# Performance work log

Hardware: AMD Instinct MI355X
Metric: run time of the kernel (lower is better)

The kernel has to match this reference:

```python
import jax, jax.numpy as jnp
import numpy as np

H = 8  # num_heads


def setup_inputs() -> dict:
    key = jax.random.key(0)
    ks = jax.random.split(key, 8)
    B, N, C = 2048, 64, 256  # B = batch(8) * nW(256) windows, N = window tokens, C = dim
    nW = 256
    return {
        "x": jax.random.normal(ks[0], (B, N, C), jnp.float32),
        "mask": jax.random.normal(ks[1], (nW, N, N), jnp.float32),
        "Wq": jax.random.normal(ks[2], (C, C), jnp.float32) * (C ** -0.5),
        "bq": jax.random.normal(ks[3], (C,), jnp.float32) * 0.02,
        "Wkv": jax.random.normal(ks[4], (C, 2 * C), jnp.float32) * (C ** -0.5),
        "bkv": jax.random.normal(ks[5], (2 * C,), jnp.float32) * 0.02,
        "Wp": jax.random.normal(ks[6], (C, C), jnp.float32) * (C ** -0.5),
        "bp": jax.random.normal(ks[7], (C,), jnp.float32) * 0.02,
    }


def reference(x, mask, Wq, bq, Wkv, bkv, Wp, bp):
    B, N, C = x.shape
    dh = C // H
    scale = dh ** -0.5
    # projections (attn_kv is None -> self-attention)
    q = (x @ Wq + bq).reshape(B, N, H, dh).transpose(0, 2, 1, 3)          # [B,H,N,dh]
    kv = (x @ Wkv + bkv).reshape(B, N, 2, H, dh).transpose(2, 0, 3, 1, 4)  # [2,B,H,N,dh]
    k, v = kv[0], kv[1]
    attn = jnp.einsum("bhqd,bhkd->bhqk", q * scale, k)                    # [B,H,N,N]
    nW = mask.shape[0]
    attn = attn.reshape(B // nW, nW, H, N, N) + mask[None, :, None]
    attn = attn.reshape(B, H, N, N)
    attn = jax.nn.softmax(attn, axis=-1)
    out = jnp.einsum("bhqk,bhkd->bhqd", attn, v)                          # [B,H,N,dh]
    out = out.transpose(0, 2, 1, 3).reshape(B, N, C)
    return out @ Wp + bp
```

## Files before the change

kernel.cpp:

```cpp
#include <hip/hip_runtime.h>

typedef __bf16 bf16v8 __attribute__((ext_vector_type(8)));
typedef bf16v8 bf16x8 __attribute__((may_alias));
typedef unsigned int u32v2 __attribute__((ext_vector_type(2)));
typedef u32v2 u32x2 __attribute__((may_alias));
typedef unsigned short u16v8 __attribute__((ext_vector_type(8)));
typedef u16v8 u16x8 __attribute__((may_alias));
typedef unsigned short u16v;
typedef u16v u16 __attribute__((may_alias));
typedef _Float16 f16v4 __attribute__((ext_vector_type(4)));
typedef f16v4 f16x4 __attribute__((may_alias));
typedef _Float16 f16v;
typedef f16v f16s __attribute__((may_alias));
typedef float f32x4 __attribute__((ext_vector_type(4)));
typedef unsigned int u32;

#define MEMFENCE() asm volatile("" ::: "memory")

union B8 { u32 u[4]; bf16v8 v; };

__device__ __forceinline__ u32 cvtpk(float lo, float hi) {
    u32 r;
    asm("v_cvt_pk_bf16_f32 %0, %1, %2" : "=v"(r) : "v"(lo), "v"(hi));
    return r;
}

__device__ __forceinline__ unsigned short f2b(float f) {
    union { float f; unsigned u; } a; a.f = f;
    unsigned r = a.u + 0x7FFFu + ((a.u >> 16) & 1u);
    return (unsigned short)(r >> 16);
}

__global__ void prep_weights(const float* __restrict__ Wq,
                             const float* __restrict__ Wkv,
                             const float* __restrict__ Wp,
                             const float* __restrict__ bq,
                             const float* __restrict__ bkv,
                             u16* __restrict__ wt,
                             u16* __restrict__ wpt,
                             float* __restrict__ b_all)
{
    int idx = blockIdx.x * 256 + threadIdx.x;
    if (idx < 196608) {
        int h  = idx / 24576;   int r  = idx % 24576;
        int m  = r / 8192;      int r2 = r % 8192;
        int tj = r2 / 4096;     int r3 = r2 % 4096;
        int ks = r3 / 512;      int r4 = r3 % 512;
        int lane = r4 >> 3, j = r4 & 7;
        int o = h * 32 + tj * 16 + (lane & 15);
        int k = ks * 32 + (lane >> 4) * 8 + j;
        float v = (m == 0) ? Wq[k * 256 + o]
                           : Wkv[k * 512 + (m == 1 ? o : 256 + o)];
        wt[idx] = f2b(v);
    } else if (idx < 262144) {
        int f  = idx - 196608;
        int h  = f / 8192;      int r2 = f % 8192;
        int tj = r2 / 4096;     int r3 = r2 % 4096;
        int ks = r3 / 512;      int r4 = r3 % 512;
        int lane = r4 >> 3, j = r4 & 7;
        int o = h * 32 + tj * 16 + (lane & 15);
        int k = ks * 32 + (lane >> 4) * 8 + j;
        wpt[f] = f2b(Wp[k * 256 + o]);
    } else if (idx < 262912) {
        int i = idx - 262144;
        b_all[i] = (i < 256) ? bq[i] : bkv[i - 256];
    }
}

__global__ __launch_bounds__(512, 2)
void qkv_proj(const float* __restrict__ x,
              const u16* __restrict__ wt,
              const float* __restrict__ b_all,
              u16* __restrict__ qkv)
{
    __shared__ __align__(16) unsigned char smem[65536];
    const int b0  = blockIdx.x * 2;
    const int tid = threadIdx.x;
    const int w   = tid >> 6;
    const int l   = tid & 63;
    const int lr  = l & 15;
    const int lg  = l >> 4;
    const int hc  = w * 32;

    f32x4 zero = {0.f, 0.f, 0.f, 0.f};

#pragma unroll
    for (int it = 0; it < 8; ++it) {
        int g   = it * 512 + tid;
        int win = g >> 11;
        int r2  = g & 2047;
        int row = r2 >> 5;
        int cg  = r2 & 31;
        const float* xb = x + (size_t)(b0 + win) * 16384;
        const float4 f0 = *(const float4*)(xb + row * 256 + cg * 8);
        const float4 f1 = *(const float4*)(xb + row * 256 + cg * 8 + 4);
        u16v8 t;
        t[0] = f2b(f0.x); t[1] = f2b(f0.y); t[2] = f2b(f0.z); t[3] = f2b(f0.w);
        t[4] = f2b(f1.x); t[5] = f2b(f1.y); t[6] = f2b(f1.z); t[7] = f2b(f1.w);
        int off = win * 32768 + row * 512 + ((cg * 16) ^ ((row & 7) << 4));
        *(u16x8*)(smem + off) = t;
    }
    __syncthreads();

    const u16* whead = wt + (size_t)w * 24576;

#pragma unroll
    for (int hf = 0; hf < 2; ++hf) {
#pragma unroll
        for (int m = 0; m < 3; ++m) {
            f32x4 acc[2][2][2];
#pragma unroll
            for (int win = 0; win < 2; ++win)
#pragma unroll
                for (int t = 0; t < 2; ++t)
#pragma unroll
                    for (int tj = 0; tj < 2; ++tj) acc[win][t][tj] = zero;
#pragma unroll
            for (int ks = 0; ks < 8; ++ks) {
                bf16v8 wf[2];
#pragma unroll
                for (int tj = 0; tj < 2; ++tj)
                    wf[tj] = *(const bf16x8*)(whead + m * 8192 + tj * 4096 + ks * 512 + l * 8);
#pragma unroll
                for (int win = 0; win < 2; ++win)
#pragma unroll
                    for (int t = 0; t < 2; ++t) {
                        int row = hf * 32 + t * 16 + lr;
                        bf16v8 af = *(const bf16x8*)(smem + win * 32768 + row * 512 +
                                                     ((ks * 64 + lg * 16) ^ ((row & 7) << 4)));
                        __builtin_amdgcn_s_setprio(1);
#pragma unroll
                        for (int tj = 0; tj < 2; ++tj)
                            acc[win][t][tj] = __builtin_amdgcn_mfma_f32_16x16x32_bf16(af, wf[tj], acc[win][t][tj], 0, 0, 0);
                        __builtin_amdgcn_s_setprio(0);
                    }
            }
#pragma unroll
            for (int win = 0; win < 2; ++win) {
                u16* base = qkv + (((size_t)(b0 + win) * 8 + w) * 3) * 2048 + m * 2048;
#pragma unroll
                for (int tj = 0; tj < 2; ++tj) {
                    float bias = b_all[m * 256 + hc + tj * 16 + lr];
#pragma unroll
                    for (int t = 0; t < 2; ++t) {
                        if (m < 2) {
#pragma unroll
                            for (int e = 0; e < 4; ++e) {
                                int tok = hf * 32 + t * 16 + lg * 4 + e;
                                base[tok * 32 + tj * 16 + lr] = f2b(acc[win][t][tj][e] + bias);
                            }
                        } else {
                            int dh   = tj * 16 + lr;
                            int tok0 = hf * 32 + t * 16 + lg * 4;
                            u32x2 pv2;
                            pv2[0] = cvtpk(acc[win][t][tj][0] + bias, acc[win][t][tj][1] + bias);
                            pv2[1] = cvtpk(acc[win][t][tj][2] + bias, acc[win][t][tj][3] + bias);
                            *(u32x2*)((unsigned char*)base + dh * 128 + tok0 * 2) = pv2;
                        }
                    }
                }
            }
        }
    }
}

__global__ __launch_bounds__(512, 4)
void attn_out(const u16* __restrict__ qkv,
              const float* __restrict__ mask,
              const u16* __restrict__ wpt,
              const float* __restrict__ bp,
              float* __restrict__ out)
{
    __shared__ __align__(16) unsigned char smem[40960];
    const int b   = blockIdx.x;
    const int wdw = b & 255;
    const int tid = threadIdx.x;
    const int w   = tid >> 6;
    const int l   = tid & 63;
    const int lr  = l & 15;
    const int lg  = l >> 4;
    const int chunk = w * 4096;
    const int moff  = 32768;
    const int hc    = w * 32;
    const float scale = 0.17677669529663687f;

    f32x4 zero = {0.f, 0.f, 0.f, 0.f};

    {
        const float* mb = mask + (size_t)wdw * 4096;
#pragma unroll
        for (int it = 0; it < 8; ++it) {
            int idx = it * 512 + tid;
            int q = idx >> 6, k = idx & 63;
            int colp = (k & 15) * 4 + (k >> 4);
            *(f16s*)(smem + moff + q * 128 + ((colp * 2) ^ ((q & 7) << 4)))
                = (_Float16)mb[idx];
        }
    }
    __syncthreads();

    const u16* qb  = qkv + (((size_t)b * 8 + w) * 3) * 2048;
    const u16* kb_ = qb + 2048;
    const unsigned char* vb = (const unsigned char*)(qb + 4096);

    bf16v8 aq[4], bk[4];
#pragma unroll
    for (int ti = 0; ti < 4; ++ti)
        aq[ti] = *(const bf16x8*)(qb + (ti * 16 + lr) * 32 + lg * 8);
#pragma unroll
    for (int tj = 0; tj < 4; ++tj)
        bk[tj] = *(const bf16x8*)(kb_ + (tj * 16 + lr) * 32 + lg * 8);

    f32x4 sH[4][4];
    __builtin_amdgcn_s_setprio(1);
#pragma unroll
    for (int ti = 0; ti < 4; ++ti)
#pragma unroll
        for (int tj = 0; tj < 4; ++tj)
            sH[ti][tj] = __builtin_amdgcn_mfma_f32_16x16x32_bf16(aq[ti], bk[tj], zero, 0, 0, 0);
    __builtin_amdgcn_s_setprio(0);

#pragma unroll
    for (int ti = 0; ti < 4; ++ti)
#pragma unroll
        for (int e = 0; e < 4; ++e) {
            int row = ti * 16 + lg * 4 + e;
            f16v4 mv = *(const f16x4*)(smem + moff + row * 128 + ((lr * 8) ^ ((row & 7) << 4)));
#pragma unroll
            for (int tj = 0; tj < 4; ++tj)
                sH[ti][tj][e] = sH[ti][tj][e] * scale + (float)mv[tj];
        }
    float inv[4][4];
#pragma unroll
    for (int ti = 0; ti < 4; ++ti)
#pragma unroll
        for (int e = 0; e < 4; ++e) {
            float v0 = sH[ti][0][e], v1 = sH[ti][1][e];
            float v2 = sH[ti][2][e], v3 = sH[ti][3][e];
            float m = fmaxf(fmaxf(v0, v1), fmaxf(v2, v3));
#pragma unroll
            for (int d = 1; d < 16; d <<= 1) m = fmaxf(m, __shfl_xor(m, d));
            v0 = __expf(v0 - m); v1 = __expf(v1 - m);
            v2 = __expf(v2 - m); v3 = __expf(v3 - m);
            float s = v0 + v1 + v2 + v3;
#pragma unroll
            for (int d = 1; d < 16; d <<= 1) s += __shfl_xor(s, d);
            inv[ti][e] = 1.0f / s;
            sH[ti][0][e] = v0; sH[ti][1][e] = v1;
            sH[ti][2][e] = v2; sH[ti][3][e] = v3;
        }
    u32 pkP[4][4][2];
#pragma unroll
    for (int ti = 0; ti < 4; ++ti)
#pragma unroll
        for (int tj = 0; tj < 4; ++tj) {
            pkP[ti][tj][0] = cvtpk(sH[ti][tj][0], sH[ti][tj][1]);
            pkP[ti][tj][1] = cvtpk(sH[ti][tj][2], sH[ti][tj][3]);
        }

    f32x4 oH[4][2];
#pragma unroll
    for (int ti = 0; ti < 4; ++ti)
#pragma unroll
        for (int tjv = 0; tjv < 2; ++tjv) oH[ti][tjv] = zero;
#pragma unroll
    for (int kb2 = 0; kb2 < 2; ++kb2) {
#pragma unroll
        for (int ti = 0; ti < 4; ++ti)
#pragma unroll
            for (int tjh = 0; tjh < 2; ++tjh) {
                int c2 = (tjh * 16 + lr) * 2;
#pragma unroll
                for (int ep = 0; ep < 2; ++ep) {
                    u32 u = pkP[ti][2 * kb2 + tjh][ep];
                    int q0 = ti * 16 + lg * 4 + ep * 2;
                    *(u16*)(smem + chunk + q0 * 64 + (c2 ^ (((q0 >> 1) & 3) << 4))) = (unsigned short)u;
                    *(u16*)(smem + chunk + (q0 + 1) * 64 + (c2 ^ ((((q0 + 1) >> 1) & 3) << 4))) = (unsigned short)(u >> 16);
                }
            }
        MEMFENCE();
        bf16v8 bv[2];
#pragma unroll
        for (int tjv = 0; tjv < 2; ++tjv) {
            int dh = tjv * 16 + lr;
            bv[tjv] = *(const bf16x8*)(vb + dh * 128 + kb2 * 64 + lg * 16);
        }
#pragma unroll
        for (int ti = 0; ti < 4; ++ti) {
            int row = ti * 16 + lr;
            bf16v8 ap = *(const bf16x8*)(smem + chunk + row * 64 + ((lg * 16) ^ (((row >> 1) & 3) << 4)));
            __builtin_amdgcn_s_setprio(1);
#pragma unroll
            for (int tjv = 0; tjv < 2; ++tjv)
                oH[ti][tjv] = __builtin_amdgcn_mfma_f32_16x16x32_bf16(ap, bv[tjv], oH[ti][tjv], 0, 0, 0);
            __builtin_amdgcn_s_setprio(0);
        }
        MEMFENCE();
    }
#pragma unroll
    for (int ti = 0; ti < 4; ++ti)
#pragma unroll
        for (int tjv = 0; tjv < 2; ++tjv)
#pragma unroll
            for (int e = 0; e < 4; ++e)
                oH[ti][tjv][e] *= inv[ti][e];

    __syncthreads();

#pragma unroll
    for (int ti = 0; ti < 4; ++ti)
#pragma unroll
        for (int tjv = 0; tjv < 2; ++tjv)
#pragma unroll
            for (int e = 0; e < 4; ++e) {
                int row = ti * 16 + lg * 4 + e;
                int cg  = hc + tjv * 16 + lr;
                *(u16*)(smem + row * 512 + ((cg * 2) ^ ((row & 7) << 4)))
                    = f2b(oH[ti][tjv][e]);
            }
    __syncthreads();

    f32x4 pacc[4][2];
#pragma unroll
    for (int ti = 0; ti < 4; ++ti)
#pragma unroll
        for (int tj = 0; tj < 2; ++tj) pacc[ti][tj] = zero;
#pragma unroll
    for (int ks = 0; ks < 8; ++ks) {
        bf16v8 a_[4];
#pragma unroll
        for (int ti = 0; ti < 4; ++ti) {
            int row = ti * 16 + lr;
            a_[ti] = *(const bf16x8*)(smem + row * 512 + ((ks * 64 + lg * 16) ^ ((row & 7) << 4)));
        }
        bf16v8 bw[2];
#pragma unroll
        for (int tj = 0; tj < 2; ++tj)
            bw[tj] = *(const bf16x8*)(wpt + (size_t)w * 8192 + tj * 4096 + ks * 512 + l * 8);
        __builtin_amdgcn_s_setprio(1);
#pragma unroll
        for (int tj = 0; tj < 2; ++tj)
#pragma unroll
            for (int ti = 0; ti < 4; ++ti)
                pacc[ti][tj] = __builtin_amdgcn_mfma_f32_16x16x32_bf16(a_[ti], bw[tj], pacc[ti][tj], 0, 0, 0);
        __builtin_amdgcn_s_setprio(0);
    }
    float* ob = out + (size_t)b * 16384;
#pragma unroll
    for (int tj = 0; tj < 2; ++tj) {
        float bias = bp[hc + tj * 16 + lr];
#pragma unroll
        for (int ti = 0; ti < 4; ++ti)
#pragma unroll
            for (int e = 0; e < 4; ++e) {
                int row = ti * 16 + lg * 4 + e;
                ob[row * 256 + hc + tj * 16 + lr] = pacc[ti][tj][e] + bias;
            }
    }
}

extern "C" void kernel_launch(void* const* d_in, const int* in_sizes, int n_in,
                              void* d_out, int out_size, void* d_ws, size_t ws_size,
                              hipStream_t stream) {
    const float* x    = (const float*)d_in[0];
    const float* mask = (const float*)d_in[1];
    const float* Wq   = (const float*)d_in[2];
    const float* bq   = (const float*)d_in[3];
    const float* Wkv  = (const float*)d_in[4];
    const float* bkv  = (const float*)d_in[5];
    const float* Wp   = (const float*)d_in[6];
    const float* bp   = (const float*)d_in[7];
    float* out = (float*)d_out;

    u16*   wt    = (u16*)d_ws;
    u16*   wpt   = wt + 196608;
    float* b_all = (float*)(wpt + 65536);

    const size_t qkv_off   = 589824;
    u16* qkv = (u16*)((unsigned char*)d_ws + qkv_off);

    prep_weights<<<1027, 256, 0, stream>>>(Wq, Wkv, Wp, bq, bkv, wt, wpt, b_all);
    qkv_proj<<<1024, 512, 0, stream>>>(x, wt, b_all, qkv);
    attn_out<<<2048, 512, 0, stream>>>(qkv, mask, wpt, bp, out);
}
```

Baseline: 202.6 us.

## Repartition QKV projection warps by token rows and keep A fragments in registers

Each warp previously owned one head and streamed all 64 token rows of both windows from shared memory. Now each warp owns 16 token rows of one window, loads its A fragments into registers once, and loops over all 8 heads, streaming weights from global or L2. This drops the repeated shared-memory A reads. In exchange each warp reads all of the weights (8x more weight traffic per block) and gets less MFMA reuse per weight fragment.

Result: slower. 261.0 us (+28.8%).

```diff
diff --git a/kernel.cpp b/kernel.cpp
--- a/kernel.cpp
+++ b/kernel.cpp
@@ -80,7 +80,6 @@
     const int l   = tid & 63;
     const int lr  = l & 15;
     const int lg  = l >> 4;
-    const int hc  = w * 32;
 
     f32x4 zero = {0.f, 0.f, 0.f, 0.f};
 
@@ -102,62 +101,57 @@
     }
     __syncthreads();
 
-    const u16* whead = wt + (size_t)w * 24576;
-
-#pragma unroll
-    for (int hf = 0; hf < 2; ++hf) {
+    const int win     = w >> 2;
+    const int tokbase = (w & 3) * 16;
+    const int xbase   = win * 32768;
+    const int rowsw   = (tokbase + lr);
+
+    bf16v8 af[8];
+#pragma unroll
+    for (int ks = 0; ks < 8; ++ks)
+        af[ks] = *(const bf16x8*)(smem + xbase + rowsw * 512 +
+                                  ((ks * 64 + lg * 16) ^ ((lr & 7) << 4)));
+
+    u16* qkvw = qkv + ((size_t)(b0 + win) * 8) * 3 * 2048;
+
+#pragma unroll
+    for (int h = 0; h < 8; ++h) {
+        const u16* whead = wt + h * 24576;
 #pragma unroll
         for (int m = 0; m < 3; ++m) {
-            f32x4 acc[2][2][2];
-#pragma unroll
-            for (int win = 0; win < 2; ++win)
-#pragma unroll
-                for (int t = 0; t < 2; ++t)
-#pragma unroll
-                    for (int tj = 0; tj < 2; ++tj) acc[win][t][tj] = zero;
+            f32x4 acc[2];
+            acc[0] = zero; acc[1] = zero;
 #pragma unroll
             for (int ks = 0; ks < 8; ++ks) {
-                bf16v8 wf[2];
-#pragma unroll
-                for (int tj = 0; tj < 2; ++tj)
-                    wf[tj] = *(const bf16x8*)(whead + m * 8192 + tj * 4096 + ks * 512 + l * 8);
-#pragma unroll
-                for (int win = 0; win < 2; ++win)
-#pragma unroll
-                    for (int t = 0; t < 2; ++t) {
-                        int row = hf * 32 + t * 16 + lr;
-                        bf16v8 af = *(const bf16x8*)(smem + win * 32768 + row * 512 +
-                                                     ((ks * 64 + lg * 16) ^ ((row & 7) << 4)));
-                        __builtin_amdgcn_s_setprio(1);
-#pragma unroll
-                        for (int tj = 0; tj < 2; ++tj)
-                            acc[win][t][tj] = __builtin_amdgcn_mfma_f32_16x16x32_bf16(af, wf[tj], acc[win][t][tj], 0, 0, 0);
-                        __builtin_amdgcn_s_setprio(0);
+                const u16* wp0 = whead + m * 8192 + ks * 512 + l * 8;
+                bf16v8 wf0 = *(const bf16x8*)(wp0);
+                bf16v8 wf1 = *(const bf16x8*)(wp0 + 4096);
+                __builtin_amdgcn_s_setprio(1);
+                acc[0] = __builtin_amdgcn_mfma_f32_16x16x32_bf16(af[ks], wf0, acc[0], 0, 0, 0);
+                acc[1] = __builtin_amdgcn_mfma_f32_16x16x32_bf16(af[ks], wf1, acc[1], 0, 0, 0);
+                __builtin_amdgcn_s_setprio(0);
+            }
+            u16* base = qkvw + h * 3 * 2048 + m * 2048;
+            if (m < 2) {
+#pragma unroll
+                for (int tj = 0; tj < 2; ++tj) {
+                    float bias = b_all[m * 256 + h * 32 + tj * 16 + lr];
+#pragma unroll
+                    for (int e = 0; e < 4; ++e) {
+                        int tok = tokbase + lg * 4 + e;
+                        base[tok * 32 + tj * 16 + lr] = f2b(acc[tj][e] + bias);
                     }
-            }
-#pragma unroll
-            for (int win = 0; win < 2; ++win) {
-                u16* base = qkv + (((size_t)(b0 + win) * 8 + w) * 3) * 2048 + m * 2048;
+                }
+            } else {
 #pragma unroll
                 for (int tj = 0; tj < 2; ++tj) {
-                    float bias = b_all[m * 256 + hc + tj * 16 + lr];
-#pragma unroll
-                    for (int t = 0; t < 2; ++t) {
-                        if (m < 2) {
-#pragma unroll
-                            for (int e = 0; e < 4; ++e) {
-                                int tok = hf * 32 + t * 16 + lg * 4 + e;
-                                base[tok * 32 + tj * 16 + lr] = f2b(acc[win][t][tj][e] + bias);
-                            }
-                        } else {
-                            int dh   = tj * 16 + lr;
-                            int tok0 = hf * 32 + t * 16 + lg * 4;
-                            u32x2 pv2;
-                            pv2[0] = cvtpk(acc[win][t][tj][0] + bias, acc[win][t][tj][1] + bias);
-                            pv2[1] = cvtpk(acc[win][t][tj][2] + bias, acc[win][t][tj][3] + bias);
-                            *(u32x2*)((unsigned char*)base + dh * 128 + tok0 * 2) = pv2;
-                        }
-                    }
+                    float bias = b_all[512 + h * 32 + tj * 16 + lr];
+                    int dh   = tj * 16 + lr;
+                    int tok0 = tokbase + lg * 4;
+                    u32x2 pv2;
+                    pv2[0] = cvtpk(acc[tj][0] + bias, acc[tj][1] + bias);
+                    pv2[1] = cvtpk(acc[tj][2] + bias, acc[tj][3] + bias);
+                    *(u32x2*)((unsigned char*)base + dh * 128 + tok0 * 2) = pv2;
                 }
             }
         }
@@ -376,7 +370,7 @@
     u16*   wpt   = wt + 196608;
     float* b_all = (float*)(wpt + 65536);
 
-    const size_t qkv_off   = 589824;
+    const size_t qkv_off = 589824;
     u16* qkv = (u16*)((unsigned char*)d_ws + qkv_off);
 
     prep_weights<<<1027, 256, 0, stream>>>(Wq, Wkv, Wp, bq, bkv, wt, wpt, b_all);
```

## Stage QKV projection output through LDS for coalesced 16-byte stores

Applied to the files above, without the earlier changes.

The qkv_proj kernel now loads the x tile in two 32-row halves instead of all 64 rows at once, cutting LDS from 64 KB to 48 KB. The freed space gives each wave a 2 KB swizzled staging area for output. Q/K results and the transposed V results are written into this area with scalar or 8-byte stores, then read back and written to global memory as contiguous 16-byte vectors. This replaces scattered 2-byte global stores, at the cost of an extra barrier between halves and extra LDS traffic. Staging relies only on compiler fences, not wave barriers, which is safe only because each wave uses its own private area.

New measurement: 213.2 us. +5.2%, slower.

```diff
diff --git a/kernel.cpp b/kernel.cpp
--- a/kernel.cpp
+++ b/kernel.cpp
@@ -4,6 +4,8 @@
 typedef bf16v8 bf16x8 __attribute__((may_alias));
 typedef unsigned int u32v2 __attribute__((ext_vector_type(2)));
 typedef u32v2 u32x2 __attribute__((may_alias));
+typedef unsigned int u32v4 __attribute__((ext_vector_type(4)));
+typedef u32v4 u32x4 __attribute__((may_alias));
 typedef unsigned short u16v8 __attribute__((ext_vector_type(8)));
 typedef u16v8 u16x8 __attribute__((may_alias));
 typedef unsigned short u16v;
@@ -73,39 +75,40 @@
               const float* __restrict__ b_all,
               u16* __restrict__ qkv)
 {
-    __shared__ __align__(16) unsigned char smem[65536];
+    __shared__ __align__(16) unsigned char smem[49152];
     const int b0  = blockIdx.x * 2;
     const int tid = threadIdx.x;
     const int w   = tid >> 6;
     const int l   = tid & 63;
     const int lr  = l & 15;
     const int lg  = l >> 4;
-    const int hc  = w * 32;
+    const int tb  = 32768 + w * 2048;
 
     f32x4 zero = {0.f, 0.f, 0.f, 0.f};
 
-#pragma unroll
-    for (int it = 0; it < 8; ++it) {
-        int g   = it * 512 + tid;
-        int win = g >> 11;
-        int r2  = g & 2047;
-        int row = r2 >> 5;
-        int cg  = r2 & 31;
-        const float* xb = x + (size_t)(b0 + win) * 16384;
-        const float4 f0 = *(const float4*)(xb + row * 256 + cg * 8);
-        const float4 f1 = *(const float4*)(xb + row * 256 + cg * 8 + 4);
-        u16v8 t;
-        t[0] = f2b(f0.x); t[1] = f2b(f0.y); t[2] = f2b(f0.z); t[3] = f2b(f0.w);
-        t[4] = f2b(f1.x); t[5] = f2b(f1.y); t[6] = f2b(f1.z); t[7] = f2b(f1.w);
-        int off = win * 32768 + row * 512 + ((cg * 16) ^ ((row & 7) << 4));
-        *(u16x8*)(smem + off) = t;
-    }
-    __syncthreads();
-
     const u16* whead = wt + (size_t)w * 24576;
 
 #pragma unroll
     for (int hf = 0; hf < 2; ++hf) {
+        if (hf) __syncthreads();
+#pragma unroll
+        for (int it = 0; it < 4; ++it) {
+            int g   = it * 512 + tid;
+            int win = g >> 10;
+            int r2  = g & 1023;
+            int rl  = r2 >> 5;
+            int cg  = r2 & 31;
+            const float* xb = x + (size_t)(b0 + win) * 16384;
+            const float4 f0 = *(const float4*)(xb + (hf * 32 + rl) * 256 + cg * 8);
+            const float4 f1 = *(const float4*)(xb + (hf * 32 + rl) * 256 + cg * 8 + 4);
+            u16v8 t;
+            t[0] = f2b(f0.x); t[1] = f2b(f0.y); t[2] = f2b(f0.z); t[3] = f2b(f0.w);
+            t[4] = f2b(f1.x); t[5] = f2b(f1.y); t[6] = f2b(f1.z); t[7] = f2b(f1.w);
+            int off = win * 16384 + rl * 512 + ((cg * 16) ^ ((rl & 7) << 4));
+            *(u16x8*)(smem + off) = t;
+        }
+        __syncthreads();
+
 #pragma unroll
         for (int m = 0; m < 3; ++m) {
             f32x4 acc[2][2][2];
@@ -125,9 +128,9 @@
                 for (int win = 0; win < 2; ++win)
 #pragma unroll
                     for (int t = 0; t < 2; ++t) {
-                        int row = hf * 32 + t * 16 + lr;
-                        bf16v8 af = *(const bf16x8*)(smem + win * 32768 + row * 512 +
-                                                     ((ks * 64 + lg * 16) ^ ((row & 7) << 4)));
+                        int rl = t * 16 + lr;
+                        bf16v8 af = *(const bf16x8*)(smem + win * 16384 + rl * 512 +
+                                                     ((ks * 64 + lg * 16) ^ ((rl & 7) << 4)));
                         __builtin_amdgcn_s_setprio(1);
 #pragma unroll
                         for (int tj = 0; tj < 2; ++tj)
@@ -138,26 +141,62 @@
 #pragma unroll
             for (int win = 0; win < 2; ++win) {
                 u16* base = qkv + (((size_t)(b0 + win) * 8 + w) * 3) * 2048 + m * 2048;
-#pragma unroll
-                for (int tj = 0; tj < 2; ++tj) {
-                    float bias = b_all[m * 256 + hc + tj * 16 + lr];
-#pragma unroll
-                    for (int t = 0; t < 2; ++t) {
-                        if (m < 2) {
+                if (m < 2) {
+#pragma unroll
+                    for (int tj = 0; tj < 2; ++tj) {
+                        float bias = b_all[m * 256 + w * 32 + tj * 16 + lr];
+                        int cb = (tj * 16 + lr) * 2;
+#pragma unroll
+                        for (int t = 0; t < 2; ++t)
 #pragma unroll
                             for (int e = 0; e < 4; ++e) {
-                                int tok = hf * 32 + t * 16 + lg * 4 + e;
-                                base[tok * 32 + tj * 16 + lr] = f2b(acc[win][t][tj][e] + bias);
+                                int tok = t * 16 + lg * 4 + e;
+                                *(u16*)(smem + tb + tok * 64 + (cb ^ (((tok >> 2) & 3) << 4)))
+                                    = f2b(acc[win][t][tj][e] + bias);
                             }
-                        } else {
-                            int dh   = tj * 16 + lr;
-                            int tok0 = hf * 32 + t * 16 + lg * 4;
+                    }
+                    MEMFENCE();
+                    {
+                        int row  = l >> 1;
+                        int half = l & 1;
+                        int swz  = ((row >> 2) & 3) << 4;
+#pragma unroll
+                        for (int j = 0; j < 2; ++j) {
+                            int cb = half * 32 + j * 16;
+                            u32v4 v = *(const u32x4*)(smem + tb + row * 64 + (cb ^ swz));
+                            *(u32x4*)((unsigned char*)base + (hf * 32 + row) * 64 + cb) = v;
+                        }
+                    }
+                    MEMFENCE();
+                } else {
+#pragma unroll
+                    for (int tj = 0; tj < 2; ++tj) {
+                        float bias = b_all[512 + w * 32 + tj * 16 + lr];
+                        int dh = tj * 16 + lr;
+                        int cb = (lg * 4) * 2;
+#pragma unroll
+                        for (int t = 0; t < 2; ++t) {
                             u32x2 pv2;
                             pv2[0] = cvtpk(acc[win][t][tj][0] + bias, acc[win][t][tj][1] + bias);
                             pv2[1] = cvtpk(acc[win][t][tj][2] + bias, acc[win][t][tj][3] + bias);
-                            *(u32x2*)((unsigned char*)base + dh * 128 + tok0 * 2) = pv2;
+                            int colb = t * 32 + cb;
+                            *(u32x2*)(smem + tb + dh * 64 + (colb ^ (((dh >> 2) & 3) << 4))) = pv2;
                         }
                     }
+                    MEMFENCE();
+                    {
+                        int dh   = l >> 1;
+                        int half = l & 1;
+                        int swz  = ((dh >> 2) & 3) << 4;
+                        unsigned char* vb = (unsigned char*)base;
+#pragma unroll
+                        for (int j = 0; j < 2; ++j) {
+                            int cb = half * 32 + j * 16;
+                            u32v4 v = *(const u32x4*)(smem + tb + dh * 64 + (cb ^ swz));
+                            *(u32x4*)(vb + dh * 128 + hf * 64 + cb) = v;
+                        }
+                    }
+                    MEMFENCE();
                 }
             }
         }
@@ -376,7 +415,7 @@
     u16*   wpt   = wt + 196608;
     float* b_all = (float*)(wpt + 65536);
 
-    const size_t qkv_off   = 589824;
+    const size_t qkv_off = 589824;
     u16* qkv = (u16*)((unsigned char*)d_ws + qkv_off);
 
     prep_weights<<<1027, 256, 0, stream>>>(Wq, Wkv, Wp, bq, bkv, wt, wpt, b_all);
```
